# Performance work log

Hardware: AMD Instinct MI355X
Metric: run time of the kernel (lower is better)

Reference implementation:

```python
import jax, jax.numpy as jnp
import numpy as np

N, E, NREL = 50000, 800000, 4
IN, EMB, HID, OUT, LVL = 32, 32, 32, 32, 3


def setup_inputs() -> dict:
    key = jax.random.key(0)
    ks = jax.random.split(key, 24)
    f32 = jnp.float32
    inp = {
        'x': jax.random.normal(ks[0], (N, IN), f32),
        'node_feat': jax.random.normal(ks[1], (N, EMB), f32),
        'edge_feat': jax.random.normal(ks[2], (E, EMB), f32),
        'src': jax.random.randint(ks[3], (E,), 0, N, jnp.int32),
        'dst': jax.random.randint(ks[4], (E,), 0, N, jnp.int32),
        'eid': jax.random.randint(ks[5], (E,), 0, NREL, jnp.int32),
        # layer 1 (in_feat=IN)
        'Wr1': jax.random.normal(ks[6], (NREL, IN + 2 * EMB, HID), f32) * 0.1,
        'attn_w1': jax.random.normal(ks[7], (EMB + HID, 1), f32) * 0.1,
        'loop_w1': jax.random.normal(ks[8], (EMB, HID), f32) * 0.1,
        'h_bias1': jax.random.normal(ks[9], (HID,), f32) * 0.1,
        'amrm_W1': jax.random.normal(ks[10], (LVL, HID, HID), f32) * 0.1,
        'amrm_b1': jax.random.normal(ks[11], (LVL, HID), f32) * 0.1,
        'amrm_a1': jax.random.normal(ks[12], (HID, 1), f32) * 0.1,
        # layer 2 (in_feat=HID)
        'Wr2': jax.random.normal(ks[13], (NREL, HID + 2 * EMB, OUT), f32) * 0.1,
        'attn_w2': jax.random.normal(ks[14], (EMB + OUT, 1), f32) * 0.1,
        'loop_w2': jax.random.normal(ks[15], (EMB, OUT), f32) * 0.1,
        'h_bias2': jax.random.normal(ks[16], (OUT,), f32) * 0.1,
        'amrm_W2': jax.random.normal(ks[17], (LVL, OUT, OUT), f32) * 0.1,
        'amrm_b2': jax.random.normal(ks[18], (LVL, OUT), f32) * 0.1,
        'amrm_a2': jax.random.normal(ks[19], (OUT, 1), f32) * 0.1,
    }
    return inp


def _rp_layer(feat, node_feat, src, dst, eid, edge_feat,
              Wr, attn_w, loop_w, h_bias, amrm_W, amrm_b, amrm_a):
    n = node_feat.shape[0]
    ones_e = jnp.ones((src.shape[0],), feat.dtype)
    # symmetric-ish degree norm: feat scaled by out-degree^-1/2
    deg_out = jnp.clip(jax.ops.segment_sum(ones_e, src, num_segments=n), 1.0)
    feat = feat * (deg_out ** -0.5)[:, None]
    # per-edge gather + relation-typed linear (grouped GEMM over NREL types)
    xe = jnp.concatenate([feat[src], edge_feat, node_feat[dst]], axis=1)  # [E, in+2*emb]
    m = jnp.zeros((xe.shape[0], Wr.shape[2]), feat.dtype)
    for r in range(Wr.shape[0]):
        m = m + jnp.where((eid == r)[:, None], xe @ Wr[r], 0.0)
    # edge attention + segment softmax over incoming edges per dst node
    z = jax.nn.leaky_relu(jnp.concatenate([node_feat[dst], m], axis=1) @ attn_w)  # [E,1]
    zmax = jax.ops.segment_max(z, dst, num_segments=n)
    ez = jnp.exp(z - zmax[dst])
    a = ez / jax.ops.segment_sum(ez, dst, num_segments=n)[dst]
    # scatter-sum aggregation
    h = jax.ops.segment_sum(a * m, dst, num_segments=n)
    h = h + node_feat @ loop_w
    deg_in = jnp.clip(jax.ops.segment_sum(ones_e, dst, num_segments=n), 1.0)
    h = h * (deg_in ** -0.5)[:, None] + h_bias
    # adaptive multi-level relation module
    lv = jax.nn.relu(jnp.einsum('nh,lho->nlo', h, amrm_W) + amrm_b[None])  # [N,L,O]
    sc = jax.nn.softmax(jnp.einsum('nlo,o->nl', lv, amrm_a[:, 0]), axis=-1)  # [N,L]
    return jnp.einsum('nl,nlo->no', sc, lv)


def reference(x, node_feat, edge_feat, src, dst, eid,
              Wr1, attn_w1, loop_w1, h_bias1, amrm_W1, amrm_b1, amrm_a1,
              Wr2, attn_w2, loop_w2, h_bias2, amrm_W2, amrm_b2, amrm_a2):
    h = jax.nn.relu(_rp_layer(x, node_feat, src, dst, eid, edge_feat,
                              Wr1, attn_w1, loop_w1, h_bias1, amrm_W1, amrm_b1, amrm_a1))
    h = jax.nn.relu(_rp_layer(h, node_feat, src, dst, eid, edge_feat,
                              Wr2, attn_w2, loop_w2, h_bias2, amrm_W2, amrm_b2, amrm_a2))
    return h
```

## Files before the change

kernel.cpp:

```cpp
#include <hip/hip_runtime.h>

#define NN 50000
#define NE 800000

#define O_DEGIN   0
#define O_DEGOUT  50048
#define O_ROWPTR  100096
#define O_CURSOR  150208
#define O_EINFO   200256
#define O_FEATN   1800256
#define O_ZF      3400256
#define O_ZNRD    3600320
#define O_VV      3800384
#define O_EZ      3800832
#define O_WDEN    4600832
#define O_YACC    5000832
#define O_H1      17800832


__global__ __launch_bounds__(256) void k_deg(const int* __restrict__ src,
                                             const int* __restrict__ dst,
                                             int* degin, int* degout) {
    int e = blockIdx.x * 256 + threadIdx.x;
    if (e < NE) {
        atomicAdd(&degin[dst[e]], 1);
        atomicAdd(&degout[src[e]], 1);
    }
}

__global__ __launch_bounds__(1024) void k_scan(const int* __restrict__ degin,
                                               int* rowptr, int* cursor) {
    __shared__ int sb[1024];
    int t = threadIdx.x;
    int carry = 0;
    for (int ch = 0; ch < 4; ch++) {
        int base = ch * 16384 + t * 16;
        int v[16];
        int s = 0;
#pragma unroll
        for (int j = 0; j < 16; j++) {
            v[j] = (base + j < NN) ? degin[base + j] : 0;
            s += v[j];
        }
        sb[t] = s;
        __syncthreads();
        for (int off = 1; off < 1024; off <<= 1) {
            int x = (t >= off) ? sb[t - off] : 0;
            __syncthreads();
            sb[t] += x;
            __syncthreads();
        }
        int excl = carry + sb[t] - s;
        int tot = sb[1023];
#pragma unroll
        for (int j = 0; j < 16; j++) {
            if (base + j < NN) { rowptr[base + j] = excl; cursor[base + j] = excl; }
            excl += v[j];
        }
        carry += tot;
        __syncthreads();
    }
    if (t == 0) rowptr[NN] = carry;
}

__global__ __launch_bounds__(256) void k_scatter(const int* __restrict__ src,
                                                 const int* __restrict__ dst,
                                                 const int* __restrict__ eid,
                                                 int* cursor, int2* einfo) {
    int e = blockIdx.x * 256 + threadIdx.x;
    if (e >= NE) return;
    int slot = atomicAdd(&cursor[dst[e]], 1);
    einfo[slot] = make_int2(src[e] | (eid[e] << 20), e);
}


__global__ __launch_bounds__(384) void k_prevec(const float* __restrict__ Wr,
                                                const float* __restrict__ attw,
                                                float* __restrict__ vvec) {
    int t = threadIdx.x;
    int r = (t >> 5) & 3, k = t & 31, part = t >> 7;
    int row = (part == 0) ? (32 + k) : (part == 1) ? k : (64 + k);
    const float* wrow = Wr + (size_t)r * 3072 + row * 32;
    float s = 0.f;
#pragma unroll
    for (int c = 0; c < 32; c++) s += wrow[c] * attw[32 + c];
    vvec[t] = s;
}

__global__ __launch_bounds__(128) void k_nodeproj(const float* __restrict__ feat,
                                                  const float* __restrict__ nfeat,
                                                  const float* __restrict__ attw,
                                                  const float* __restrict__ vvec,
                                                  const int* __restrict__ degout,
                                                  float* __restrict__ featn,
                                                  float* __restrict__ zF,
                                                  float* __restrict__ znrd) {
    int n = blockIdx.x * 128 + threadIdx.x;
    if (n >= NN) return;
    int dg = degout[n];
    float sc0 = rsqrtf((float)(dg > 1 ? dg : 1));
    const float* fin = feat + (size_t)n * 32;
    const float* nin = nfeat + (size_t)n * 32;
    float fv[32], nv[32];
#pragma unroll
    for (int k = 0; k < 32; k += 4) {
        float4 f4 = *(const float4*)&fin[k];
        fv[k] = f4.x * sc0; fv[k + 1] = f4.y * sc0;
        fv[k + 2] = f4.z * sc0; fv[k + 3] = f4.w * sc0;
        float4 n4 = *(const float4*)&nin[k];
        nv[k] = n4.x; nv[k + 1] = n4.y; nv[k + 2] = n4.z; nv[k + 3] = n4.w;
    }
    float* fo = featn + (size_t)n * 32;
#pragma unroll
    for (int k = 0; k < 32; k += 4)
        *(float4*)&fo[k] = make_float4(fv[k], fv[k + 1], fv[k + 2], fv[k + 3]);
    float zn = 0.f;
#pragma unroll
    for (int k = 0; k < 32; k++) zn += nv[k] * attw[k];
#pragma unroll
    for (int r = 0; r < 4; r++) {
        float zf = 0.f, zd = 0.f;
        const float* vf = vvec + 128 + r * 32;
        const float* vd = vvec + 256 + r * 32;
#pragma unroll
        for (int k = 0; k < 32; k++) { zf += fv[k] * vf[k]; zd += nv[k] * vd[k]; }
        zF[r * NN + n] = zf;
        znrd[r * NN + n] = zn + zd;
    }
}

__global__ __launch_bounds__(256) void k_ez(const int* __restrict__ src,
                                            const int* __restrict__ dst,
                                            const int* __restrict__ eid,
                                            const float* __restrict__ efeat,
                                            const float* __restrict__ zF,
                                            const float* __restrict__ znrd,
                                            const float* __restrict__ vvec,
                                            float* __restrict__ ez) {
    int e = blockIdx.x * 256 + threadIdx.x;
    int s = src[e], d = dst[e], r = eid[e];
    const float* er = efeat + (size_t)e * 32;
    float d0 = 0.f, d1 = 0.f, d2 = 0.f, d3 = 0.f;
#pragma unroll
    for (int k = 0; k < 32; k += 4) {
        float4 f = *(const float4*)&er[k];
        d0 += f.x * vvec[k]       + f.y * vvec[k + 1]
            + f.z * vvec[k + 2]   + f.w * vvec[k + 3];
        d1 += f.x * vvec[32 + k]  + f.y * vvec[33 + k]
            + f.z * vvec[34 + k]  + f.w * vvec[35 + k];
        d2 += f.x * vvec[64 + k]  + f.y * vvec[65 + k]
            + f.z * vvec[66 + k]  + f.w * vvec[67 + k];
        d3 += f.x * vvec[96 + k]  + f.y * vvec[97 + k]
            + f.z * vvec[98 + k]  + f.w * vvec[99 + k];
    }
    float dot = (r == 0) ? d0 : (r == 1) ? d1 : (r == 2) ? d2 : d3;
    float z = znrd[r * NN + d] + zF[r * NN + s] + dot;
    z = z > 0.f ? z : 0.01f * z;
    ez[e] = __expf(z);
}

__global__ __launch_bounds__(512) void k_agg(const int* __restrict__ rowptr,
                                             const int2* __restrict__ einfo,
                                             const float* __restrict__ ez,
                                             const float* __restrict__ efeat,
                                             const float* __restrict__ featn,
                                             float* __restrict__ yacc,
                                             float* __restrict__ wden) {
    int tid = threadIdx.x;
    int lane = tid & 63;
    int n = blockIdx.x * 8 + (tid >> 6);
    int c = lane & 31;
    int p = lane >> 5;

    int rp0 = rowptr[n];
    int deg = rowptr[n + 1] - rp0;

    float yf0 = 0.f, yf1 = 0.f, yf2 = 0.f, yf3 = 0.f;
    float ye0 = 0.f, ye1 = 0.f, ye2 = 0.f, ye3 = 0.f;
    float w0 = 0.f, w1 = 0.f, w2 = 0.f, w3 = 0.f, den = 0.f;

    for (int t = p; t < deg; t += 2) {
        int2 me = einfo[rp0 + t];
        int sb = me.x & 0xFFFFF;
        int rb = me.x >> 20;
        float ezv = ez[me.y];
        float ef = efeat[(size_t)me.y * 32 + c];
        float fn = featn[(size_t)sb * 32 + c];
        float e0 = (rb == 0) ? ezv : 0.f;
        float e1 = (rb == 1) ? ezv : 0.f;
        float e2 = (rb == 2) ? ezv : 0.f;
        float e3 = (rb == 3) ? ezv : 0.f;
        yf0 += e0 * fn; yf1 += e1 * fn; yf2 += e2 * fn; yf3 += e3 * fn;
        ye0 += e0 * ef; ye1 += e1 * ef; ye2 += e2 * ef; ye3 += e3 * ef;
        w0 += e0; w1 += e1; w2 += e2; w3 += e3;
        den += ezv;
    }

    yf0 += __shfl_xor(yf0, 32); yf1 += __shfl_xor(yf1, 32);
    yf2 += __shfl_xor(yf2, 32); yf3 += __shfl_xor(yf3, 32);
    ye0 += __shfl_xor(ye0, 32); ye1 += __shfl_xor(ye1, 32);
    ye2 += __shfl_xor(ye2, 32); ye3 += __shfl_xor(ye3, 32);
    w0 += __shfl_xor(w0, 32); w1 += __shfl_xor(w1, 32);
    w2 += __shfl_xor(w2, 32); w3 += __shfl_xor(w3, 32);
    den += __shfl_xor(den, 32);

    float* yo = yacc + (size_t)n * 256 + p * 128 + c;
    yo[0]  = p ? ye0 : yf0;
    yo[32] = p ? ye1 : yf1;
    yo[64] = p ? ye2 : yf2;
    yo[96] = p ? ye3 : yf3;
    if (lane < 5) {
        float wv = (lane == 0) ? w0 : (lane == 1) ? w1 : (lane == 2) ? w2
                 : (lane == 3) ? w3 : den;
        wden[n * 8 + lane] = wv;
    }
}

__global__ __launch_bounds__(128) void k_post(const int* __restrict__ rowptr,
                                              const float* __restrict__ yacc,
                                              const float* __restrict__ wden,
                                              const float* __restrict__ nfeat,
                                              const float* __restrict__ Wr,
                                              const float* __restrict__ lw,
                                              const float* __restrict__ hbias,
                                              const float* __restrict__ aW,
                                              const float* __restrict__ ab,
                                              const float* __restrict__ aa,
                                              float* __restrict__ out) {
    int n = blockIdx.x * 128 + threadIdx.x;
    if (n >= NN) return;
    int deg = rowptr[n + 1] - rowptr[n];
    float den = wden[n * 8 + 4];
    float invden = (deg > 0) ? 1.f / den : 0.f;
    const float* u = yacc + (size_t)n * 256;
    const float* nf = nfeat + (size_t)n * 32;

    float nv[32];
#pragma unroll
    for (int k = 0; k < 32; k += 4) {
        float4 f4 = *(const float4*)&nf[k];
        nv[k] = f4.x; nv[k + 1] = f4.y; nv[k + 2] = f4.z; nv[k + 3] = f4.w;
    }

    float acc[32];
#pragma unroll
    for (int i = 0; i < 32; i++) acc[i] = 0.f;
    for (int r = 0; r < 4; r++) {
        const float* W = Wr + (size_t)r * 3072;
        float wr = wden[n * 8 + r];
        const float* uf = u + r * 32;
        const float* ue = u + 128 + r * 32;
        for (int k4 = 0; k4 < 32; k4 += 4) {
            float4 a4 = *(const float4*)&uf[k4];
            float4 b4 = *(const float4*)&ue[k4];
            float g0 = wr * nv[k4],     g1 = wr * nv[k4 + 1];
            float g2 = wr * nv[k4 + 2], g3 = wr * nv[k4 + 3];
            const float* Wk = W + k4 * 32;
#pragma unroll
            for (int i = 0; i < 32; i++)
                acc[i] += a4.x * Wk[i]        + a4.y * Wk[32 + i]
                        + a4.z * Wk[64 + i]   + a4.w * Wk[96 + i]
                        + b4.x * Wk[1024 + i] + b4.y * Wk[1056 + i]
                        + b4.z * Wk[1088 + i] + b4.w * Wk[1120 + i]
                        + g0 * Wk[2048 + i]   + g1 * Wk[2080 + i]
                        + g2 * Wk[2112 + i]   + g3 * Wk[2144 + i];
        }
    }

    float hsc = rsqrtf((float)(deg > 1 ? deg : 1));
    float h[32];
#pragma unroll
    for (int i = 0; i < 32; i++) h[i] = acc[i] * invden;
    for (int k4 = 0; k4 < 32; k4 += 4) {
        const float* Lk = lw + k4 * 32;
#pragma unroll
        for (int i = 0; i < 32; i++)
            h[i] += nv[k4] * Lk[i] + nv[k4 + 1] * Lk[32 + i]
                  + nv[k4 + 2] * Lk[64 + i] + nv[k4 + 3] * Lk[96 + i];
    }
#pragma unroll
    for (int i = 0; i < 32; i++) h[i] = h[i] * hsc + hbias[i];

    float s[3];
#pragma unroll
    for (int l = 0; l < 3; l++) {
        const float* A = aW + (size_t)l * 1024;
#pragma unroll
        for (int i = 0; i < 32; i++) acc[i] = ab[l * 32 + i];
        for (int k4 = 0; k4 < 32; k4 += 4) {
            const float* Ak = A + k4 * 32;
#pragma unroll
            for (int i = 0; i < 32; i++)
                acc[i] += h[k4] * Ak[i] + h[k4 + 1] * Ak[32 + i]
                        + h[k4 + 2] * Ak[64 + i] + h[k4 + 3] * Ak[96 + i];
        }
        float sl = 0.f;
#pragma unroll
        for (int i = 0; i < 32; i++) {
            float lv = acc[i] > 0.f ? acc[i] : 0.f;
            sl += lv * aa[i];
        }
        s[l] = sl;
    }
    float mx = fmaxf(s[0], fmaxf(s[1], s[2]));
    float e0 = __expf(s[0] - mx), e1 = __expf(s[1] - mx), e2 = __expf(s[2] - mx);
    float inv = 1.f / (e0 + e1 + e2);
    float scl[3] = {e0 * inv, e1 * inv, e2 * inv};

    float outv[32];
#pragma unroll
    for (int i = 0; i < 32; i++) outv[i] = 0.f;
#pragma unroll
    for (int l = 0; l < 3; l++) {
        const float* A = aW + (size_t)l * 1024;
#pragma unroll
        for (int i = 0; i < 32; i++) acc[i] = ab[l * 32 + i];
        for (int k4 = 0; k4 < 32; k4 += 4) {
            const float* Ak = A + k4 * 32;
#pragma unroll
            for (int i = 0; i < 32; i++)
                acc[i] += h[k4] * Ak[i] + h[k4 + 1] * Ak[32 + i]
                        + h[k4 + 2] * Ak[64 + i] + h[k4 + 3] * Ak[96 + i];
        }
#pragma unroll
        for (int i = 0; i < 32; i++) {
            float lv = acc[i] > 0.f ? acc[i] : 0.f;
            outv[i] += scl[l] * lv;
        }
    }
    float* op = out + (size_t)n * 32;
#pragma unroll
    for (int i = 0; i < 32; i += 4)
        *(float4*)&op[i] = make_float4(fmaxf(outv[i], 0.f), fmaxf(outv[i + 1], 0.f),
                                       fmaxf(outv[i + 2], 0.f), fmaxf(outv[i + 3], 0.f));
}


static void launch_layer(const float* feat, const float* nf, const float* efeat,
                         const int* src, const int* dst, const int* eid,
                         const float* Wr, const float* attw, const float* lw,
                         const float* hb, const float* aW, const float* ab,
                         const float* aa, float* wsf, int* wsi, float* out,
                         hipStream_t stream) {
    k_prevec<<<1, 384, 0, stream>>>(Wr, attw, wsf + O_VV);
    k_nodeproj<<<391, 128, 0, stream>>>(feat, nf, attw, wsf + O_VV, wsi + O_DEGOUT,
                                        wsf + O_FEATN, wsf + O_ZF, wsf + O_ZNRD);
    k_ez<<<3125, 256, 0, stream>>>(src, dst, eid, efeat, wsf + O_ZF, wsf + O_ZNRD,
                                   wsf + O_VV, wsf + O_EZ);
    k_agg<<<6250, 512, 0, stream>>>(wsi + O_ROWPTR, (const int2*)(wsi + O_EINFO),
                                    wsf + O_EZ, efeat, wsf + O_FEATN,
                                    wsf + O_YACC, wsf + O_WDEN);
    k_post<<<391, 128, 0, stream>>>(wsi + O_ROWPTR, wsf + O_YACC, wsf + O_WDEN,
                                    nf, Wr, lw, hb, aW, ab, aa, out);
}

extern "C" void kernel_launch(void* const* d_in, const int* in_sizes, int n_in,
                              void* d_out, int out_size, void* d_ws, size_t ws_size,
                              hipStream_t stream) {
    const float* x     = (const float*)d_in[0];
    const float* nfeat = (const float*)d_in[1];
    const float* efeat = (const float*)d_in[2];
    const int*   src   = (const int*)d_in[3];
    const int*   dst   = (const int*)d_in[4];
    const int*   eid   = (const int*)d_in[5];
    const float* Wr1   = (const float*)d_in[6];
    const float* attw1 = (const float*)d_in[7];
    const float* lw1   = (const float*)d_in[8];
    const float* hb1   = (const float*)d_in[9];
    const float* aW1   = (const float*)d_in[10];
    const float* ab1   = (const float*)d_in[11];
    const float* aa1   = (const float*)d_in[12];
    const float* Wr2   = (const float*)d_in[13];
    const float* attw2 = (const float*)d_in[14];
    const float* lw2   = (const float*)d_in[15];
    const float* hb2   = (const float*)d_in[16];
    const float* aW2   = (const float*)d_in[17];
    const float* ab2   = (const float*)d_in[18];
    const float* aa2   = (const float*)d_in[19];

    float* wsf = (float*)d_ws;
    int*   wsi = (int*)d_ws;
    float* out = (float*)d_out;

    hipMemsetAsync(d_ws, 0, (size_t)O_ROWPTR * 4, stream);

    k_deg<<<NE / 256, 256, 0, stream>>>(src, dst, wsi + O_DEGIN, wsi + O_DEGOUT);
    k_scan<<<1, 1024, 0, stream>>>(wsi + O_DEGIN, wsi + O_ROWPTR, wsi + O_CURSOR);
    k_scatter<<<NE / 256, 256, 0, stream>>>(src, dst, eid, wsi + O_CURSOR,
                                            (int2*)(wsi + O_EINFO));

    launch_layer(x, nfeat, efeat, src, dst, eid, Wr1, attw1, lw1, hb1, aW1, ab1, aa1,
                 wsf, wsi, wsf + O_H1, stream);
    launch_layer(wsf + O_H1, nfeat, efeat, src, dst, eid, Wr2, attw2, lw2, hb2,
                 aW2, ab2, aa2, wsf, wsi, out, stream);
}
```

Before: 731.5 us.

## Transpose aggregation outputs to feature-major layout and prefetch edges in aggregation

The aggregation kernel now stages its per-node accumulators through shared memory and writes them feature-major (yaccT, wdenT), and node features are also written transposed. The post kernel then reads them with coalesced per-thread column loads instead of strided row loads. The edge loop in aggregation is software-pipelined to prefetch the next edge's gathers, and the degree scan uses wave shuffles instead of a barrier-heavy shared-memory scan. The costs are extra shared memory, a block barrier in aggregation, and an additional transposed copy of node features.

```diff
diff --git a/kernel.cpp b/kernel.cpp
--- a/kernel.cpp
+++ b/kernel.cpp
@@ -13,9 +13,10 @@
 #define O_ZNRD    3600320
 #define O_VV      3800384
 #define O_EZ      3800832
-#define O_WDEN    4600832
-#define O_YACC    5000832
-#define O_H1      17800832
+#define O_NFT     4600832
+#define O_WDENT   6200832
+#define O_YACCT   6450880
+#define O_H1      19250880
 
 
 __global__ __launch_bounds__(256) void k_deg(const int* __restrict__ src,
@@ -30,8 +31,10 @@
 
 __global__ __launch_bounds__(1024) void k_scan(const int* __restrict__ degin,
                                                int* rowptr, int* cursor) {
-    __shared__ int sb[1024];
+    __shared__ int swsum[16];
+    __shared__ int stot;
     int t = threadIdx.x;
+    int lane = t & 63, w = t >> 6;
     int carry = 0;
     for (int ch = 0; ch < 4; ch++) {
         int base = ch * 16384 + t * 16;
@@ -42,22 +45,33 @@
             v[j] = (base + j < NN) ? degin[base + j] : 0;
             s += v[j];
         }
-        sb[t] = s;
+        int incl = s;
+#pragma unroll
+        for (int off = 1; off < 64; off <<= 1) {
+            int x = __shfl_up(incl, off, 64);
+            if (lane >= off) incl += x;
+        }
+        if (lane == 63) swsum[w] = incl;
         __syncthreads();
-        for (int off = 1; off < 1024; off <<= 1) {
-            int x = (t >= off) ? sb[t - off] : 0;
-            __syncthreads();
-            sb[t] += x;
-            __syncthreads();
-        }
-        int excl = carry + sb[t] - s;
-        int tot = sb[1023];
+        if (w == 0) {
+            int y = (lane < 16) ? swsum[lane] : 0;
+            int yi = y;
+#pragma unroll
+            for (int off = 1; off < 16; off <<= 1) {
+                int x = __shfl_up(yi, off, 64);
+                if (lane >= off) yi += x;
+            }
+            if (lane < 16) swsum[lane] = yi - y;
+            if (lane == 15) stot = yi;
+        }
+        __syncthreads();
+        int excl = carry + swsum[w] + (incl - s);
 #pragma unroll
         for (int j = 0; j < 16; j++) {
             if (base + j < NN) { rowptr[base + j] = excl; cursor[base + j] = excl; }
             excl += v[j];
         }
-        carry += tot;
+        carry += stot;
         __syncthreads();
     }
     if (t == 0) rowptr[NN] = carry;
@@ -93,6 +107,7 @@
                                                   const float* __restrict__ vvec,
                                                   const int* __restrict__ degout,
                                                   float* __restrict__ featn,
+                                                  float* __restrict__ nfT,
                                                   float* __restrict__ zF,
                                                   float* __restrict__ znrd) {
     int n = blockIdx.x * 128 + threadIdx.x;
@@ -114,6 +129,8 @@
 #pragma unroll
     for (int k = 0; k < 32; k += 4)
         *(float4*)&fo[k] = make_float4(fv[k], fv[k + 1], fv[k + 2], fv[k + 3]);
+#pragma unroll
+    for (int k = 0; k < 32; k++) nfT[(size_t)k * NN + n] = nv[k];
     float zn = 0.f;
 #pragma unroll
     for (int k = 0; k < 32; k++) zn += nv[k] * attw[k];
@@ -164,11 +181,14 @@
                                              const float* __restrict__ ez,
                                              const float* __restrict__ efeat,
                                              const float* __restrict__ featn,
-                                             float* __restrict__ yacc,
-                                             float* __restrict__ wden) {
+                                             float* __restrict__ yaccT,
+                                             float* __restrict__ wdenT) {
+    __shared__ float sT[256 * 9];
     int tid = threadIdx.x;
     int lane = tid & 63;
-    int n = blockIdx.x * 8 + (tid >> 6);
+    int wid = tid >> 6;
+    int n0 = blockIdx.x * 8;
+    int n = n0 + wid;
     int c = lane & 31;
     int p = lane >> 5;
 
@@ -179,21 +199,35 @@
     float ye0 = 0.f, ye1 = 0.f, ye2 = 0.f, ye3 = 0.f;
     float w0 = 0.f, w1 = 0.f, w2 = 0.f, w3 = 0.f, den = 0.f;
 
+    int2 meA = make_int2(0, 0), meB = make_int2(0, 0);
+    float ezA = 0.f, efA = 0.f, fnA = 0.f;
+    if (p < deg) {
+        meA = einfo[rp0 + p];
+        ezA = ez[meA.y];
+        efA = efeat[(size_t)meA.y * 32 + c];
+        fnA = featn[(size_t)(meA.x & 0xFFFFF) * 32 + c];
+    }
+    if (p + 2 < deg) meB = einfo[rp0 + p + 2];
+
     for (int t = p; t < deg; t += 2) {
-        int2 me = einfo[rp0 + t];
-        int sb = me.x & 0xFFFFF;
-        int rb = me.x >> 20;
-        float ezv = ez[me.y];
-        float ef = efeat[(size_t)me.y * 32 + c];
-        float fn = featn[(size_t)sb * 32 + c];
-        float e0 = (rb == 0) ? ezv : 0.f;
-        float e1 = (rb == 1) ? ezv : 0.f;
-        float e2 = (rb == 2) ? ezv : 0.f;
-        float e3 = (rb == 3) ? ezv : 0.f;
-        yf0 += e0 * fn; yf1 += e1 * fn; yf2 += e2 * fn; yf3 += e3 * fn;
-        ye0 += e0 * ef; ye1 += e1 * ef; ye2 += e2 * ef; ye3 += e3 * ef;
+        float ezB = 0.f, efB = 0.f, fnB = 0.f;
+        int2 meC = make_int2(0, 0);
+        if (t + 2 < deg) {
+            ezB = ez[meB.y];
+            efB = efeat[(size_t)meB.y * 32 + c];
+            fnB = featn[(size_t)(meB.x & 0xFFFFF) * 32 + c];
+        }
+        if (t + 4 < deg) meC = einfo[rp0 + t + 4];
+        int rb = meA.x >> 20;
+        float e0 = (rb == 0) ? ezA : 0.f;
+        float e1 = (rb == 1) ? ezA : 0.f;
+        float e2 = (rb == 2) ? ezA : 0.f;
+        float e3 = (rb == 3) ? ezA : 0.f;
+        yf0 += e0 * fnA; yf1 += e1 * fnA; yf2 += e2 * fnA; yf3 += e3 * fnA;
+        ye0 += e0 * efA; ye1 += e1 * efA; ye2 += e2 * efA; ye3 += e3 * efA;
         w0 += e0; w1 += e1; w2 += e2; w3 += e3;
-        den += ezv;
+        den += ezA;
+        meA = meB; ezA = ezB; efA = efB; fnA = fnB; meB = meC;
     }
 
     yf0 += __shfl_xor(yf0, 32); yf1 += __shfl_xor(yf1, 32);
@@ -204,22 +238,30 @@
     w2 += __shfl_xor(w2, 32); w3 += __shfl_xor(w3, 32);
     den += __shfl_xor(den, 32);
 
-    float* yo = yacc + (size_t)n * 256 + p * 128 + c;
-    yo[0]  = p ? ye0 : yf0;
-    yo[32] = p ? ye1 : yf1;
-    yo[64] = p ? ye2 : yf2;
-    yo[96] = p ? ye3 : yf3;
     if (lane < 5) {
         float wv = (lane == 0) ? w0 : (lane == 1) ? w1 : (lane == 2) ? w2
                  : (lane == 3) ? w3 : den;
-        wden[n * 8 + lane] = wv;
-    }
-}
-
-__global__ __launch_bounds__(128) void k_post(const int* __restrict__ rowptr,
-                                              const float* __restrict__ yacc,
-                                              const float* __restrict__ wden,
-                                              const float* __restrict__ nfeat,
+        wdenT[lane * NN + n] = wv;
+    }
+
+    {
+        int kb = 128 * p + c;
+        sT[(kb +  0) * 9 + wid] = p ? ye0 : yf0;
+        sT[(kb + 32) * 9 + wid] = p ? ye1 : yf1;
+        sT[(kb + 64) * 9 + wid] = p ? ye2 : yf2;
+        sT[(kb + 96) * 9 + wid] = p ? ye3 : yf3;
+    }
+    __syncthreads();
+    int k = tid >> 1, hf = tid & 1;
+    float4 v = make_float4(sT[k * 9 + hf * 4 + 0], sT[k * 9 + hf * 4 + 1],
+                           sT[k * 9 + hf * 4 + 2], sT[k * 9 + hf * 4 + 3]);
+    *(float4*)&yaccT[(size_t)k * NN + n0 + hf * 4] = v;
+}
+
+__global__ __launch_bounds__(256) void k_post(const int* __restrict__ rowptr,
+                                              const float* __restrict__ yaccT,
+                                              const float* __restrict__ wdenT,
+                                              const float* __restrict__ nfT,
                                               const float* __restrict__ Wr,
                                               const float* __restrict__ lw,
                                               const float* __restrict__ hbias,
@@ -227,43 +269,41 @@
                                               const float* __restrict__ ab,
                                               const float* __restrict__ aa,
                                               float* __restrict__ out) {
-    int n = blockIdx.x * 128 + threadIdx.x;
+    int n = blockIdx.x * 256 + threadIdx.x;
     if (n >= NN) return;
     int deg = rowptr[n + 1] - rowptr[n];
-    float den = wden[n * 8 + 4];
+    float den = wdenT[4 * NN + n];
     float invden = (deg > 0) ? 1.f / den : 0.f;
-    const float* u = yacc + (size_t)n * 256;
-    const float* nf = nfeat + (size_t)n * 32;
 
     float nv[32];
 #pragma unroll
-    for (int k = 0; k < 32; k += 4) {
-        float4 f4 = *(const float4*)&nf[k];
-        nv[k] = f4.x; nv[k + 1] = f4.y; nv[k + 2] = f4.z; nv[k + 3] = f4.w;
-    }
+    for (int k = 0; k < 32; k++) nv[k] = nfT[(size_t)k * NN + n];
 
     float acc[32];
 #pragma unroll
     for (int i = 0; i < 32; i++) acc[i] = 0.f;
+#pragma unroll
     for (int r = 0; r < 4; r++) {
         const float* W = Wr + (size_t)r * 3072;
-        float wr = wden[n * 8 + r];
-        const float* uf = u + r * 32;
-        const float* ue = u + 128 + r * 32;
+        float wr = wdenT[r * NN + n];
+        const float* ufc = yaccT + (size_t)(r * 32) * NN + n;
+        const float* uec = yaccT + (size_t)(128 + r * 32) * NN + n;
         for (int k4 = 0; k4 < 32; k4 += 4) {
-            float4 a4 = *(const float4*)&uf[k4];
-            float4 b4 = *(const float4*)&ue[k4];
+            float a0 = ufc[(size_t)(k4 + 0) * NN], a1 = ufc[(size_t)(k4 + 1) * NN];
+            float a2 = ufc[(size_t)(k4 + 2) * NN], a3 = ufc[(size_t)(k4 + 3) * NN];
+            float b0 = uec[(size_t)(k4 + 0) * NN], b1 = uec[(size_t)(k4 + 1) * NN];
+            float b2 = uec[(size_t)(k4 + 2) * NN], b3 = uec[(size_t)(k4 + 3) * NN];
             float g0 = wr * nv[k4],     g1 = wr * nv[k4 + 1];
             float g2 = wr * nv[k4 + 2], g3 = wr * nv[k4 + 3];
             const float* Wk = W + k4 * 32;
 #pragma unroll
             for (int i = 0; i < 32; i++)
-                acc[i] += a4.x * Wk[i]        + a4.y * Wk[32 + i]
-                        + a4.z * Wk[64 + i]   + a4.w * Wk[96 + i]
-                        + b4.x * Wk[1024 + i] + b4.y * Wk[1056 + i]
-                        + b4.z * Wk[1088 + i] + b4.w * Wk[1120 + i]
-                        + g0 * Wk[2048 + i]   + g1 * Wk[2080 + i]
-                        + g2 * Wk[2112 + i]   + g3 * Wk[2144 + i];
+                acc[i] += a0 * Wk[i]        + a1 * Wk[32 + i]
+                        + a2 * Wk[64 + i]   + a3 * Wk[96 + i]
+                        + b0 * Wk[1024 + i] + b1 * Wk[1056 + i]
+                        + b2 * Wk[1088 + i] + b3 * Wk[1120 + i]
+                        + g0 * Wk[2048 + i] + g1 * Wk[2080 + i]
+                        + g2 * Wk[2112 + i] + g3 * Wk[2144 + i];
         }
     }
 
@@ -344,14 +384,15 @@
                          hipStream_t stream) {
     k_prevec<<<1, 384, 0, stream>>>(Wr, attw, wsf + O_VV);
     k_nodeproj<<<391, 128, 0, stream>>>(feat, nf, attw, wsf + O_VV, wsi + O_DEGOUT,
-                                        wsf + O_FEATN, wsf + O_ZF, wsf + O_ZNRD);
+                                        wsf + O_FEATN, wsf + O_NFT,
+                                        wsf + O_ZF, wsf + O_ZNRD);
     k_ez<<<3125, 256, 0, stream>>>(src, dst, eid, efeat, wsf + O_ZF, wsf + O_ZNRD,
                                    wsf + O_VV, wsf + O_EZ);
     k_agg<<<6250, 512, 0, stream>>>(wsi + O_ROWPTR, (const int2*)(wsi + O_EINFO),
                                     wsf + O_EZ, efeat, wsf + O_FEATN,
-                                    wsf + O_YACC, wsf + O_WDEN);
-    k_post<<<391, 128, 0, stream>>>(wsi + O_ROWPTR, wsf + O_YACC, wsf + O_WDEN,
-                                    nf, Wr, lw, hb, aW, ab, aa, out);
+                                    wsf + O_YACCT, wsf + O_WDENT);
+    k_post<<<196, 256, 0, stream>>>(wsi + O_ROWPTR, wsf + O_YACCT, wsf + O_WDENT,
+                                    wsf + O_NFT, Wr, lw, hb, aW, ab, aa, out);
 }
 
 extern "C" void kernel_launch(void* const* d_in, const int* in_sizes, int n_in,
```

Result: slower. 761.2 us (+4.1%).
